# Kernel optimization log

Hardware: AMD Instinct MI355X
Metric: run time of the kernel (lower is better)

The kernel has to match this reference:

```python
import jax, jax.numpy as jnp
import numpy as np

B, S, D = 2, 2048, 2048
H, KV = 32, 8
HD = D // H          # 64
REP = H // KV        # 4


def setup_inputs() -> dict:
    key = jax.random.key(0)
    ks = jax.random.split(key, 7)
    x = jax.random.normal(ks[0], (B, S, D), dtype=jnp.float32)
    # rotary tables: cos/sin of position*inv_freq, shape (S, HD//2)
    inv_freq = 1.0 / (10000.0 ** (np.arange(0, HD, 2, dtype=np.float32) / HD))
    t = np.arange(S, dtype=np.float32)
    freqs = np.outer(t, inv_freq)
    freqs_cos = jnp.asarray(np.cos(freqs))
    freqs_sin = jnp.asarray(np.sin(freqs))
    sc = 0.02
    wq = jax.random.normal(ks[1], (D, D), dtype=jnp.float32) * sc
    wk = jax.random.normal(ks[2], (KV * HD, D), dtype=jnp.float32) * sc
    wv = jax.random.normal(ks[3], (KV * HD, D), dtype=jnp.float32) * sc
    wo = jax.random.normal(ks[4], (D, D), dtype=jnp.float32) * sc
    return {"x": x, "freqs_cos": freqs_cos, "freqs_sin": freqs_sin,
            "wq": wq, "wk": wk, "wv": wv, "wo": wo}


def _rope(t, cos, sin):
    # t: (B, S, h, HD); interleaved real/imag pairs along last dim
    r = t[..., 0::2]
    i = t[..., 1::2]
    cos = cos[None, :, None, :]
    sin = sin[None, :, None, :]
    out_r = r * cos - i * sin
    out_i = r * sin + i * cos
    return jnp.stack([out_r, out_i], axis=-1).reshape(t.shape)


def reference(x, freqs_cos, freqs_sin, wq, wk, wv, wo):
    b, s, d = x.shape
    xq = jnp.einsum('bsd,ed->bse', x, wq).reshape(b, s, H, HD)
    xk = jnp.einsum('bsd,ed->bse', x, wk).reshape(b, s, KV, HD)
    xv = jnp.einsum('bsd,ed->bse', x, wv).reshape(b, s, KV, HD)
    xq = _rope(xq, freqs_cos, freqs_sin)
    xk = _rope(xk, freqs_cos, freqs_sin)
    # GQA repeat_kv: (B,S,KV,HD) -> (B,S,H,HD)
    xk = jnp.repeat(xk, REP, axis=2)
    xv = jnp.repeat(xv, REP, axis=2)
    # to (B,H,S,HD)
    q = xq.transpose(0, 2, 1, 3)
    k = xk.transpose(0, 2, 1, 3)
    v = xv.transpose(0, 2, 1, 3)
    scores = jnp.einsum('bhqd,bhkd->bhqk', q, k) / jnp.sqrt(jnp.float32(HD))
    causal = jnp.tril(jnp.ones((s, s), dtype=bool))
    scores = jnp.where(causal[None, None], scores, jnp.float32(-1e30))
    probs = jax.nn.softmax(scores, axis=-1)
    out = jnp.einsum('bhqk,bhkd->bhqd', probs, v)
    out = out.transpose(0, 2, 1, 3).reshape(b, s, d)
    return jnp.einsum('bsd,ed->bse', out, wo)
```

## Files before the change

### kernel.cpp

```cpp
#include <hip/hip_runtime.h>
#include <cstdint>
#include <cstddef>

#define S_LEN 2048
#define D_MODEL 2048
#define NH 32
#define NKV 8
#define HD_ 64
#define BATCH 2
#define KVD 512
#define MTOT 4096

typedef float f32x4 __attribute__((ext_vector_type(4)));
typedef short s16x8 __attribute__((ext_vector_type(8)));
typedef unsigned int u32;
typedef unsigned int u32x4 __attribute__((ext_vector_type(4)));

__device__ __forceinline__ unsigned short f2bf(float f) {
  unsigned int u = __builtin_bit_cast(unsigned int, f);
  u = (u + 0x7fffu + ((u >> 16) & 1u)) >> 16;
  return (unsigned short)u;
}
__device__ __forceinline__ float bf2f(unsigned short h) {
  return __builtin_bit_cast(float, ((unsigned int)h) << 16);
}
__device__ __forceinline__ float fexp2(float x) {
#if __has_builtin(__builtin_amdgcn_exp2f)
  return __builtin_amdgcn_exp2f(x);
#else
  return exp2f(x);
#endif
}

__device__ __forceinline__ void gl_lds16(const void* g, void* l) {
  __builtin_amdgcn_global_load_lds((const __attribute__((address_space(1))) u32*)g,
                                   (__attribute__((address_space(3))) u32*)l, 16, 0, 0);
}

__global__ void cvt_kernel(const float* __restrict__ in, unsigned short* __restrict__ out, int n4) {
  int i = blockIdx.x * blockDim.x + threadIdx.x;
  if (i >= n4) return;
  float4 v = reinterpret_cast<const float4*>(in)[i];
  ushort4 o;
  o.x = f2bf(v.x); o.y = f2bf(v.y); o.z = f2bf(v.z); o.w = f2bf(v.w);
  reinterpret_cast<ushort4*>(out)[i] = o;
}

__global__ void cvt4_kernel(const float* __restrict__ a, const float* __restrict__ b,
                            const float* __restrict__ c, const float* __restrict__ d,
                            unsigned short* __restrict__ oa, unsigned short* __restrict__ ob,
                            unsigned short* __restrict__ oc, unsigned short* __restrict__ od,
                            int na4, int nb4, int nc4, int nd4) {
  int j = blockIdx.x * blockDim.x + threadIdx.x;
  const float* src; unsigned short* dst;
  if (j < na4) { src = a; dst = oa; }
  else {
    j -= na4;
    if (j < nb4) { src = b; dst = ob; }
    else {
      j -= nb4;
      if (j < nc4) { src = c; dst = oc; }
      else {
        j -= nc4;
        if (j >= nd4) return;
        src = d; dst = od;
      }
    }
  }
  float4 v = reinterpret_cast<const float4*>(src)[j];
  ushort4 o;
  o.x = f2bf(v.x); o.y = f2bf(v.y); o.z = f2bf(v.z); o.w = f2bf(v.w);
  reinterpret_cast<ushort4*>(dst)[j] = o;
}

__global__ void rope2_kernel(unsigned short* __restrict__ qb, unsigned short* __restrict__ kb,
                             const float* __restrict__ cosb, const float* __restrict__ sinb,
                             int totq, int totk, float qscale) {
  int i = blockIdx.x * blockDim.x + threadIdx.x;
  unsigned short* buf; int nheads; float scale;
  if (i < totq) { buf = qb; nheads = NH; scale = qscale; }
  else {
    i -= totq;
    if (i >= totk) return;
    buf = kb; nheads = NKV; scale = 1.0f;
  }
  int pair = i & 31;
  int rest = i >> 5;
  int s = (rest / nheads) % S_LEN;
  float c = cosb[s * 32 + pair], sn = sinb[s * 32 + pair];
  size_t base = (size_t)rest * HD_ + (size_t)pair * 2;
  float r  = bf2f(buf[base]);
  float im = bf2f(buf[base + 1]);
  buf[base]     = f2bf((r * c - im * sn) * scale);
  buf[base + 1] = f2bf((r * sn + im * c) * scale);
}

template<int MODE>
__global__ __launch_bounds__(256) void gemm_bt(const unsigned short* __restrict__ A,
                                               const unsigned short* __restrict__ W,
                                               float* __restrict__ Cf,
                                               unsigned short* __restrict__ Cb,
                                               int M, int N, int K) {
  __shared__ alignas(16) short As[128 * 32];
  __shared__ alignas(16) short Bs[128 * 32];
  int tid = threadIdx.x;
  int lane = tid & 63, wid = tid >> 6;
  int m0 = blockIdx.y * 128;
  int n0 = blockIdx.x * 128;
  int wm = (wid >> 1) * 64, wn = (wid & 1) * 64;
  int lrow = lane & 15, lkk = lane >> 4;
  int srow = lane >> 2;
  int scb  = (lane & 3) * 16;
  f32x4 acc[4][4] = {};

  for (int k0 = 0; k0 < K; k0 += 32) {
    __syncthreads();
#pragma unroll
    for (int i = 0; i < 2; ++i) {
      int c = wid * 2 + i;
      int row = c * 16 + srow;
      const char* ga = (const char*)A + ((size_t)(m0 + row) * K + k0) * 2 + scb;
      gl_lds16(ga, (char*)As + c * 1024);
      const char* gw = (const char*)W + ((size_t)(n0 + row) * K + k0) * 2 + scb;
      gl_lds16(gw, (char*)Bs + c * 1024);
    }
    __syncthreads();
    s16x8 af[4], bfr[4];
#pragma unroll
    for (int mi = 0; mi < 4; ++mi) {
      int row = wm + mi * 16 + lrow;
      af[mi] = *reinterpret_cast<const s16x8*>((const char*)As + row * 64 + lkk * 16);
    }
#pragma unroll
    for (int ni = 0; ni < 4; ++ni) {
      int row = wn + ni * 16 + lrow;
      bfr[ni] = *reinterpret_cast<const s16x8*>((const char*)Bs + row * 64 + lkk * 16);
    }
#pragma unroll
    for (int mi = 0; mi < 4; ++mi)
#pragma unroll
      for (int ni = 0; ni < 4; ++ni)
        acc[mi][ni] = __builtin_amdgcn_mfma_f32_16x16x32_bf16(af[mi], bfr[ni], acc[mi][ni], 0, 0, 0);
  }

#pragma unroll
  for (int mi = 0; mi < 4; ++mi)
#pragma unroll
    for (int ni = 0; ni < 4; ++ni)
#pragma unroll
      for (int r = 0; r < 4; ++r) {
        int row = m0 + wm + mi * 16 + lkk * 4 + r;
        int col = n0 + wn + ni * 16 + lrow;
        if (MODE == 1) Cf[(size_t)row * N + col] = acc[mi][ni][r];
        else           Cb[(size_t)row * N + col] = f2bf(acc[mi][ni][r]);
      }
}

__global__ __launch_bounds__(256) void gemm_kv(const unsigned short* __restrict__ A,
                                               const unsigned short* __restrict__ Wk,
                                               const unsigned short* __restrict__ Wv,
                                               unsigned short* __restrict__ Ck,
                                               unsigned short* __restrict__ Cvt,
                                               int M, int K) {
  __shared__ alignas(16) short As[128 * 32];
  __shared__ alignas(16) short Bs[128 * 32];
  int tid = threadIdx.x;
  int lane = tid & 63, wid = tid >> 6;
  bool isV = blockIdx.x >= 4;
  const unsigned short* W = isV ? Wv : Wk;
  int n0 = (isV ? (int)blockIdx.x - 4 : (int)blockIdx.x) * 128;
  int m0 = blockIdx.y * 128;
  int wm = (wid >> 1) * 64, wn = (wid & 1) * 64;
  int lrow = lane & 15, lkk = lane >> 4;
  int srow = lane >> 2;
  int scb  = (lane & 3) * 16;
  f32x4 acc[4][4] = {};

  for (int k0 = 0; k0 < K; k0 += 32) {
    __syncthreads();
#pragma unroll
    for (int i = 0; i < 2; ++i) {
      int c = wid * 2 + i;
      int row = c * 16 + srow;
      const char* ga = (const char*)A + ((size_t)(m0 + row) * K + k0) * 2 + scb;
      gl_lds16(ga, (char*)As + c * 1024);
      const char* gw = (const char*)W + ((size_t)(n0 + row) * K + k0) * 2 + scb;
      gl_lds16(gw, (char*)Bs + c * 1024);
    }
    __syncthreads();
    s16x8 af[4], bfr[4];
#pragma unroll
    for (int mi = 0; mi < 4; ++mi) {
      int row = wm + mi * 16 + lrow;
      af[mi] = *reinterpret_cast<const s16x8*>((const char*)As + row * 64 + lkk * 16);
    }
#pragma unroll
    for (int ni = 0; ni < 4; ++ni) {
      int row = wn + ni * 16 + lrow;
      bfr[ni] = *reinterpret_cast<const s16x8*>((const char*)Bs + row * 64 + lkk * 16);
    }
#pragma unroll
    for (int mi = 0; mi < 4; ++mi)
#pragma unroll
      for (int ni = 0; ni < 4; ++ni)
        acc[mi][ni] = __builtin_amdgcn_mfma_f32_16x16x32_bf16(af[mi], bfr[ni], acc[mi][ni], 0, 0, 0);
  }

  if (!isV) {
#pragma unroll
    for (int mi = 0; mi < 4; ++mi)
#pragma unroll
      for (int ni = 0; ni < 4; ++ni)
#pragma unroll
        for (int r = 0; r < 4; ++r) {
          int row = m0 + wm + mi * 16 + lkk * 4 + r;
          int col = n0 + wn + ni * 16 + lrow;
          Ck[(size_t)row * KVD + col] = f2bf(acc[mi][ni][r]);
        }
  } else {
#pragma unroll
    for (int mi = 0; mi < 4; ++mi)
#pragma unroll
      for (int ni = 0; ni < 4; ++ni) {
        int col = n0 + wn + ni * 16 + lrow;
        int mrow = m0 + wm + mi * 16 + lkk * 4;
        ushort4 o;
        o.x = f2bf(acc[mi][ni][0]); o.y = f2bf(acc[mi][ni][1]);
        o.z = f2bf(acc[mi][ni][2]); o.w = f2bf(acc[mi][ni][3]);
        *reinterpret_cast<ushort4*>(Cvt + (size_t)col * M + mrow) = o;
      }
  }
}

__global__ __launch_bounds__(256) void attn_kernel(const unsigned short* __restrict__ Q,
                                                   const unsigned short* __restrict__ Kb,
                                                   const unsigned short* __restrict__ Vt,
                                                   unsigned short* __restrict__ O) {
  __shared__ alignas(16) short Ks[2][64 * 64];
  __shared__ alignas(16) short Vs[2][64 * 64];

  int tid = threadIdx.x, lane = tid & 63, wid = tid >> 6;
  int qi = lane & 15, lk = lane >> 4;
  int bh = blockIdx.y;
  int b = bh / NH, h = bh % NH, kvh = h >> 2;
  size_t bS = (size_t)b * S_LEN;
  int srow = tid >> 3;
  int scb  = (tid & 7) * 16;
  int sw0  = (srow & 7) << 4;

  const char* kbG = (const char*)Kb + (bS * KVD + (size_t)kvh * HD_) * 2;
  const char* vtG = (const char*)Vt + ((size_t)(kvh * 64) * MTOT + bS) * 2;

  s16x8 kr0, kr1, vr0, vr1;
  auto GLOAD = [&](int kv0) {
    kr0 = *reinterpret_cast<const s16x8*>(kbG + (size_t)(kv0 + srow) * (KVD * 2) + scb);
    kr1 = *reinterpret_cast<const s16x8*>(kbG + (size_t)(kv0 + srow + 32) * (KVD * 2) + scb);
    vr0 = *reinterpret_cast<const s16x8*>(vtG + (size_t)srow * (MTOT * 2) + kv0 * 2 + scb);
    vr1 = *reinterpret_cast<const s16x8*>(vtG + (size_t)(srow + 32) * (MTOT * 2) + kv0 * 2 + scb);
  };
  auto SWRITE = [&](int bf) {
    *reinterpret_cast<s16x8*>((char*)Ks[bf] + srow * 128 + (scb ^ sw0)) = kr0;
    *reinterpret_cast<s16x8*>((char*)Ks[bf] + (srow + 32) * 128 + (scb ^ sw0)) = kr1;
    *reinterpret_cast<s16x8*>((char*)Vs[bf] + srow * 128 + (scb ^ sw0)) = vr0;
    *reinterpret_cast<s16x8*>((char*)Vs[bf] + (srow + 32) * 128 + (scb ^ sw0)) = vr1;
  };

#pragma unroll 1
  for (int job = 0; job < 2; ++job) {
    int qtile = (job == 0) ? (int)blockIdx.x : 31 - (int)blockIdx.x;
    int q0 = qtile * 64;
    int nt = qtile + 1;

    const unsigned short* qptr = Q + (bS + q0 + wid * 16 + qi) * D_MODEL + h * HD_;
    s16x8 qf0 = *reinterpret_cast<const s16x8*>(qptr + lk * 8);
    s16x8 qf1 = *reinterpret_cast<const s16x8*>(qptr + 32 + lk * 8);

    f32x4 o_acc[4] = {};
    float m_run = -3.0e38f, l_run = 0.f;

    GLOAD(0);
    SWRITE(0);
    __syncthreads();
    int cur = 0;

    for (int t = 0; t < nt; ++t) {
      if (t + 1 < nt) GLOAD((t + 1) * 64);

      const char* kbase = (const char*)Ks[cur];
      const char* vbase = (const char*)Vs[cur];

      f32x4 st[4];
      __builtin_amdgcn_s_setprio(1);
#pragma unroll
      for (int mt = 0; mt < 4; ++mt) {
        int row = mt * 16 + qi;
        int sw = (row & 7) << 4;
        s16x8 ka0 = *reinterpret_cast<const s16x8*>(kbase + row * 128 + ((lk * 16) ^ sw));
        s16x8 ka1 = *reinterpret_cast<const s16x8*>(kbase + row * 128 + ((64 + lk * 16) ^ sw));
        f32x4 a = {};
        a = __builtin_amdgcn_mfma_f32_16x16x32_bf16(ka0, qf0, a, 0, 0, 0);
        a = __builtin_amdgcn_mfma_f32_16x16x32_bf16(ka1, qf1, a, 0, 0, 0);
        st[mt] = a;
      }
      __builtin_amdgcn_s_setprio(0);

      if (t == nt - 1) {
        int ql = wid * 16 + qi;
#pragma unroll
        for (int mt = 0; mt < 4; ++mt)
#pragma unroll
          for (int r = 0; r < 4; ++r) {
            int kvl = mt * 16 + 4 * lk + r;
            if (kvl > ql) st[mt][r] = -3.0e38f;
          }
      }

      float pmax = st[0][0];
#pragma unroll
      for (int mt = 0; mt < 4; ++mt)
#pragma unroll
        for (int r = 0; r < 4; ++r) pmax = fmaxf(pmax, st[mt][r]);
      pmax = fmaxf(pmax, __shfl_xor(pmax, 16, 64));
      pmax = fmaxf(pmax, __shfl_xor(pmax, 32, 64));
      float mnew = fmaxf(m_run, pmax);
      float alpha = fexp2(m_run - mnew);
      m_run = mnew;
      float psum = 0.f;
#pragma unroll
      for (int mt = 0; mt < 4; ++mt)
#pragma unroll
        for (int r = 0; r < 4; ++r) {
          float p = fexp2(st[mt][r] - mnew);
          st[mt][r] = p;
          psum += p;
        }
      psum += __shfl_xor(psum, 16, 64);
      psum += __shfl_xor(psum, 32, 64);
      l_run = l_run * alpha + psum;

      u32 pk[4][2];
#pragma unroll
      for (int mt = 0; mt < 4; ++mt)
#pragma unroll
        for (int w = 0; w < 2; ++w)
          pk[mt][w] = (u32)f2bf(st[mt][2 * w]) | ((u32)f2bf(st[mt][2 * w + 1]) << 16);

      float ar[4];
#pragma unroll
      for (int r = 0; r < 4; ++r) ar[r] = __shfl(alpha, 4 * lk + r, 64);
#pragma unroll
      for (int n = 0; n < 4; ++n)
#pragma unroll
        for (int r = 0; r < 4; ++r) o_acc[n][r] *= ar[r];

      int s0 = qi + 32 * (lk & 1);
      int s2 = s0 + 16;
      bool hiw = lk >= 2;
      s16x8 pa[2];
#pragma unroll
      for (int ks = 0; ks < 2; ++ks) {
        u32 a0 = (u32)__shfl((int)pk[2 * ks][0], s0, 64), b0 = (u32)__shfl((int)pk[2 * ks + 1][0], s0, 64);
        u32 a1 = (u32)__shfl((int)pk[2 * ks][1], s0, 64), b1 = (u32)__shfl((int)pk[2 * ks + 1][1], s0, 64);
        u32 a2 = (u32)__shfl((int)pk[2 * ks][0], s2, 64), b2 = (u32)__shfl((int)pk[2 * ks + 1][0], s2, 64);
        u32 a3 = (u32)__shfl((int)pk[2 * ks][1], s2, 64), b3 = (u32)__shfl((int)pk[2 * ks + 1][1], s2, 64);
        u32x4 wv_;
        wv_[0] = hiw ? b0 : a0; wv_[1] = hiw ? b1 : a1;
        wv_[2] = hiw ? b2 : a2; wv_[3] = hiw ? b3 : a3;
        pa[ks] = __builtin_bit_cast(s16x8, wv_);
      }

      __builtin_amdgcn_s_setprio(1);
#pragma unroll
      for (int n = 0; n < 4; ++n) {
        int vr = n * 16 + qi;
        int sw = (vr & 7) << 4;
        s16x8 vb0 = *reinterpret_cast<const s16x8*>(vbase + vr * 128 + ((lk * 16) ^ sw));
        s16x8 vb1 = *reinterpret_cast<const s16x8*>(vbase + vr * 128 + ((64 + lk * 16) ^ sw));
        o_acc[n] = __builtin_amdgcn_mfma_f32_16x16x32_bf16(pa[0], vb0, o_acc[n], 0, 0, 0);
        o_acc[n] = __builtin_amdgcn_mfma_f32_16x16x32_bf16(pa[1], vb1, o_acc[n], 0, 0, 0);
      }
      __builtin_amdgcn_s_setprio(0);

      if (t + 1 < nt) SWRITE(cur ^ 1);
      __syncthreads();
      cur ^= 1;
    }

    float linv[4];
#pragma unroll
    for (int r = 0; r < 4; ++r) linv[r] = 1.0f / __shfl(l_run, 4 * lk + r, 64);
#pragma unroll
    for (int n = 0; n < 4; ++n)
#pragma unroll
      for (int r = 0; r < 4; ++r) {
        size_t row = bS + q0 + wid * 16 + 4 * lk + r;
        int col = h * HD_ + n * 16 + qi;
        O[row * D_MODEL + col] = f2bf(o_acc[n][r] * linv[r]);
      }
  }
}

extern "C" void kernel_launch(void* const* d_in, const int* in_sizes, int n_in,
                              void* d_out, int out_size, void* d_ws, size_t ws_size,
                              hipStream_t stream) {
  const float* x  = (const float*)d_in[0];
  const float* fc = (const float*)d_in[1];
  const float* fs = (const float*)d_in[2];
  const float* wq = (const float*)d_in[3];
  const float* wk = (const float*)d_in[4];
  const float* wv = (const float*)d_in[5];
  const float* wo = (const float*)d_in[6];
  float* out = (float*)d_out;

  const size_t nx  = (size_t)BATCH * S_LEN * D_MODEL;
  const size_t nw  = (size_t)D_MODEL * D_MODEL;
  const size_t nwk = (size_t)KVD * D_MODEL;
  const size_t nkv = (size_t)BATCH * S_LEN * KVD;

  char* ws = (char*)d_ws;
  unsigned short* xb  = (unsigned short*)ws;  ws += nx  * 2;
  unsigned short* wqb = (unsigned short*)ws;  ws += nw  * 2;
  unsigned short* wkb = (unsigned short*)ws;  ws += nwk * 2;
  unsigned short* wvb = (unsigned short*)ws;  ws += nwk * 2;
  unsigned short* wob = (unsigned short*)ws;  ws += nw  * 2;
  unsigned short* qb  = (unsigned short*)ws;  ws += nx  * 2;
  unsigned short* kb  = (unsigned short*)ws;  ws += nkv * 2;
  unsigned short* vtb = (unsigned short*)ws;  ws += nkv * 2;
  unsigned short* ab  = (unsigned short*)ws;  ws += nx  * 2;

  cvt_kernel<<<dim3((nx / 4 + 255) / 256), dim3(256), 0, stream>>>(x, xb, nx / 4);
  {
    int na4 = nw / 4, nb4 = nwk / 4, nc4 = nwk / 4, nd4 = nw / 4;
    int tot = na4 + nb4 + nc4 + nd4;
    cvt4_kernel<<<dim3((tot + 255) / 256), dim3(256), 0, stream>>>(wq, wk, wv, wo, wqb, wkb, wvb, wob,
                                                                   na4, nb4, nc4, nd4);
  }

  const int M = BATCH * S_LEN;
  gemm_bt<0><<<dim3(D_MODEL / 128, M / 128), dim3(256), 0, stream>>>(xb, wqb, nullptr, qb, M, D_MODEL, D_MODEL);
  gemm_kv<<<dim3(8, M / 128), dim3(256), 0, stream>>>(xb, wkb, wvb, kb, vtb, M, D_MODEL);

  {
    int totq = BATCH * S_LEN * NH * 32;
    int totk = BATCH * S_LEN * NKV * 32;
    rope2_kernel<<<dim3((totq + totk + 255) / 256), dim3(256), 0, stream>>>(qb, kb, fc, fs, totq, totk,
                                                                            0.18033688011112042f);
  }

  attn_kernel<<<dim3(16, BATCH * NH), dim3(256), 0, stream>>>(qb, kb, vtb, ab);

  gemm_bt<1><<<dim3(D_MODEL / 128, M / 128), dim3(256), 0, stream>>>(ab, wob, out, nullptr, M, D_MODEL, D_MODEL);
}
```

Baseline: 392.4 us.

## Fuse QKV GEMMs and enlarge attention query tiles with lazy rescaling

Merges the Q projection and the K/V projection GEMMs into a single launch with 24 column-block groups. The attention kernel moves to 512 threads per block and 128-row query tiles, so each K/V tile loaded into shared memory serves twice as many queries, while warps skip tiles that lie entirely past their causal limit. It also adds a lazy online-softmax rescale that only updates the running max when it grows by more than a threshold. The risks are higher register and occupancy pressure from the larger blocks, warp divergence at the diagonal, and subtle numerical effects from the deferred rescaling.

Result: faster. 336.3 us (-14.3%).

```diff
diff --git a/kernel.cpp b/kernel.cpp
--- a/kernel.cpp
+++ b/kernel.cpp
@@ -95,12 +95,92 @@
   buf[base + 1] = f2bf((r * sn + im * c) * scale);
 }
 
-template<int MODE>
-__global__ __launch_bounds__(256) void gemm_bt(const unsigned short* __restrict__ A,
-                                               const unsigned short* __restrict__ W,
-                                               float* __restrict__ Cf,
-                                               unsigned short* __restrict__ Cb,
-                                               int M, int N, int K) {
+__global__ __launch_bounds__(256) void gemm_qkv(const unsigned short* __restrict__ A,
+                                                const unsigned short* __restrict__ Wq,
+                                                const unsigned short* __restrict__ Wk,
+                                                const unsigned short* __restrict__ Wv,
+                                                unsigned short* __restrict__ Cq,
+                                                unsigned short* __restrict__ Ck,
+                                                unsigned short* __restrict__ Cvt,
+                                                int M, int K) {
+  __shared__ alignas(16) short As[128 * 32];
+  __shared__ alignas(16) short Bs[128 * 32];
+  int tid = threadIdx.x;
+  int lane = tid & 63, wid = tid >> 6;
+  int bx = blockIdx.x;
+  const unsigned short* W; int n0, mode;
+  if (bx < 16)      { W = Wq; n0 = bx * 128;        mode = 0; }
+  else if (bx < 20) { W = Wk; n0 = (bx - 16) * 128; mode = 1; }
+  else              { W = Wv; n0 = (bx - 20) * 128; mode = 2; }
+  int m0 = blockIdx.y * 128;
+  int wm = (wid >> 1) * 64, wn = (wid & 1) * 64;
+  int lrow = lane & 15, lkk = lane >> 4;
+  int srow = lane >> 2;
+  int scb  = (lane & 3) * 16;
+  f32x4 acc[4][4] = {};
+
+  for (int k0 = 0; k0 < K; k0 += 32) {
+    __syncthreads();
+#pragma unroll
+    for (int i = 0; i < 2; ++i) {
+      int c = wid * 2 + i;
+      int row = c * 16 + srow;
+      const char* ga = (const char*)A + ((size_t)(m0 + row) * K + k0) * 2 + scb;
+      gl_lds16(ga, (char*)As + c * 1024);
+      const char* gw = (const char*)W + ((size_t)(n0 + row) * K + k0) * 2 + scb;
+      gl_lds16(gw, (char*)Bs + c * 1024);
+    }
+    __syncthreads();
+    s16x8 af[4], bfr[4];
+#pragma unroll
+    for (int mi = 0; mi < 4; ++mi) {
+      int row = wm + mi * 16 + lrow;
+      af[mi] = *reinterpret_cast<const s16x8*>((const char*)As + row * 64 + lkk * 16);
+    }
+#pragma unroll
+    for (int ni = 0; ni < 4; ++ni) {
+      int row = wn + ni * 16 + lrow;
+      bfr[ni] = *reinterpret_cast<const s16x8*>((const char*)Bs + row * 64 + lkk * 16);
+    }
+#pragma unroll
+    for (int mi = 0; mi < 4; ++mi)
+#pragma unroll
+      for (int ni = 0; ni < 4; ++ni)
+        acc[mi][ni] = __builtin_amdgcn_mfma_f32_16x16x32_bf16(af[mi], bfr[ni], acc[mi][ni], 0, 0, 0);
+  }
+
+  if (mode == 2) {
+#pragma unroll
+    for (int mi = 0; mi < 4; ++mi)
+#pragma unroll
+      for (int ni = 0; ni < 4; ++ni) {
+        int col = n0 + wn + ni * 16 + lrow;
+        int mrow = m0 + wm + mi * 16 + lkk * 4;
+        ushort4 o;
+        o.x = f2bf(acc[mi][ni][0]); o.y = f2bf(acc[mi][ni][1]);
+        o.z = f2bf(acc[mi][ni][2]); o.w = f2bf(acc[mi][ni][3]);
+        *reinterpret_cast<ushort4*>(Cvt + (size_t)col * M + mrow) = o;
+      }
+  } else {
+    unsigned short* C = (mode == 0) ? Cq : Ck;
+    int N = (mode == 0) ? D_MODEL : KVD;
+#pragma unroll
+    for (int mi = 0; mi < 4; ++mi)
+#pragma unroll
+      for (int ni = 0; ni < 4; ++ni)
+#pragma unroll
+        for (int r = 0; r < 4; ++r) {
+          int row = m0 + wm + mi * 16 + lkk * 4 + r;
+          int col = n0 + wn + ni * 16 + lrow;
+          C[(size_t)row * N + col] = f2bf(acc[mi][ni][r]);
+        }
+  }
+}
+
+__global__ __launch_bounds__(256) void gemm_out(const unsigned short* __restrict__ A,
+                                                const unsigned short* __restrict__ W,
+                                                float* __restrict__ Cf,
+                                                int M, int N, int K) {
   __shared__ alignas(16) short As[128 * 32];
   __shared__ alignas(16) short Bs[128 * 32];
   int tid = threadIdx.x;
@@ -151,88 +231,11 @@
       for (int r = 0; r < 4; ++r) {
         int row = m0 + wm + mi * 16 + lkk * 4 + r;
         int col = n0 + wn + ni * 16 + lrow;
-        if (MODE == 1) Cf[(size_t)row * N + col] = acc[mi][ni][r];
-        else           Cb[(size_t)row * N + col] = f2bf(acc[mi][ni][r]);
+        Cf[(size_t)row * N + col] = acc[mi][ni][r];
       }
 }
 
-__global__ __launch_bounds__(256) void gemm_kv(const unsigned short* __restrict__ A,
-                                               const unsigned short* __restrict__ Wk,
-                                               const unsigned short* __restrict__ Wv,
-                                               unsigned short* __restrict__ Ck,
-                                               unsigned short* __restrict__ Cvt,
-                                               int M, int K) {
-  __shared__ alignas(16) short As[128 * 32];
-  __shared__ alignas(16) short Bs[128 * 32];
-  int tid = threadIdx.x;
-  int lane = tid & 63, wid = tid >> 6;
-  bool isV = blockIdx.x >= 4;
-  const unsigned short* W = isV ? Wv : Wk;
-  int n0 = (isV ? (int)blockIdx.x - 4 : (int)blockIdx.x) * 128;
-  int m0 = blockIdx.y * 128;
-  int wm = (wid >> 1) * 64, wn = (wid & 1) * 64;
-  int lrow = lane & 15, lkk = lane >> 4;
-  int srow = lane >> 2;
-  int scb  = (lane & 3) * 16;
-  f32x4 acc[4][4] = {};
-
-  for (int k0 = 0; k0 < K; k0 += 32) {
-    __syncthreads();
-#pragma unroll
-    for (int i = 0; i < 2; ++i) {
-      int c = wid * 2 + i;
-      int row = c * 16 + srow;
-      const char* ga = (const char*)A + ((size_t)(m0 + row) * K + k0) * 2 + scb;
-      gl_lds16(ga, (char*)As + c * 1024);
-      const char* gw = (const char*)W + ((size_t)(n0 + row) * K + k0) * 2 + scb;
-      gl_lds16(gw, (char*)Bs + c * 1024);
-    }
-    __syncthreads();
-    s16x8 af[4], bfr[4];
-#pragma unroll
-    for (int mi = 0; mi < 4; ++mi) {
-      int row = wm + mi * 16 + lrow;
-      af[mi] = *reinterpret_cast<const s16x8*>((const char*)As + row * 64 + lkk * 16);
-    }
-#pragma unroll
-    for (int ni = 0; ni < 4; ++ni) {
-      int row = wn + ni * 16 + lrow;
-      bfr[ni] = *reinterpret_cast<const s16x8*>((const char*)Bs + row * 64 + lkk * 16);
-    }
-#pragma unroll
-    for (int mi = 0; mi < 4; ++mi)
-#pragma unroll
-      for (int ni = 0; ni < 4; ++ni)
-        acc[mi][ni] = __builtin_amdgcn_mfma_f32_16x16x32_bf16(af[mi], bfr[ni], acc[mi][ni], 0, 0, 0);
-  }
-
-  if (!isV) {
-#pragma unroll
-    for (int mi = 0; mi < 4; ++mi)
-#pragma unroll
-      for (int ni = 0; ni < 4; ++ni)
-#pragma unroll
-        for (int r = 0; r < 4; ++r) {
-          int row = m0 + wm + mi * 16 + lkk * 4 + r;
-          int col = n0 + wn + ni * 16 + lrow;
-          Ck[(size_t)row * KVD + col] = f2bf(acc[mi][ni][r]);
-        }
-  } else {
-#pragma unroll
-    for (int mi = 0; mi < 4; ++mi)
-#pragma unroll
-      for (int ni = 0; ni < 4; ++ni) {
-        int col = n0 + wn + ni * 16 + lrow;
-        int mrow = m0 + wm + mi * 16 + lkk * 4;
-        ushort4 o;
-        o.x = f2bf(acc[mi][ni][0]); o.y = f2bf(acc[mi][ni][1]);
-        o.z = f2bf(acc[mi][ni][2]); o.w = f2bf(acc[mi][ni][3]);
-        *reinterpret_cast<ushort4*>(Cvt + (size_t)col * M + mrow) = o;
-      }
-  }
-}
-
-__global__ __launch_bounds__(256) void attn_kernel(const unsigned short* __restrict__ Q,
+__global__ __launch_bounds__(512) void attn_kernel(const unsigned short* __restrict__ Q,
                                                    const unsigned short* __restrict__ Kb,
                                                    const unsigned short* __restrict__ Vt,
                                                    unsigned short* __restrict__ O) {
@@ -251,25 +254,22 @@
   const char* kbG = (const char*)Kb + (bS * KVD + (size_t)kvh * HD_) * 2;
   const char* vtG = (const char*)Vt + ((size_t)(kvh * 64) * MTOT + bS) * 2;
 
-  s16x8 kr0, kr1, vr0, vr1;
+  s16x8 kr, vr;
   auto GLOAD = [&](int kv0) {
-    kr0 = *reinterpret_cast<const s16x8*>(kbG + (size_t)(kv0 + srow) * (KVD * 2) + scb);
-    kr1 = *reinterpret_cast<const s16x8*>(kbG + (size_t)(kv0 + srow + 32) * (KVD * 2) + scb);
-    vr0 = *reinterpret_cast<const s16x8*>(vtG + (size_t)srow * (MTOT * 2) + kv0 * 2 + scb);
-    vr1 = *reinterpret_cast<const s16x8*>(vtG + (size_t)(srow + 32) * (MTOT * 2) + kv0 * 2 + scb);
+    kr = *reinterpret_cast<const s16x8*>(kbG + (size_t)(kv0 + srow) * (KVD * 2) + scb);
+    vr = *reinterpret_cast<const s16x8*>(vtG + (size_t)srow * (MTOT * 2) + kv0 * 2 + scb);
   };
   auto SWRITE = [&](int bf) {
-    *reinterpret_cast<s16x8*>((char*)Ks[bf] + srow * 128 + (scb ^ sw0)) = kr0;
-    *reinterpret_cast<s16x8*>((char*)Ks[bf] + (srow + 32) * 128 + (scb ^ sw0)) = kr1;
-    *reinterpret_cast<s16x8*>((char*)Vs[bf] + srow * 128 + (scb ^ sw0)) = vr0;
-    *reinterpret_cast<s16x8*>((char*)Vs[bf] + (srow + 32) * 128 + (scb ^ sw0)) = vr1;
+    *reinterpret_cast<s16x8*>((char*)Ks[bf] + srow * 128 + (scb ^ sw0)) = kr;
+    *reinterpret_cast<s16x8*>((char*)Vs[bf] + srow * 128 + (scb ^ sw0)) = vr;
   };
 
 #pragma unroll 1
   for (int job = 0; job < 2; ++job) {
-    int qtile = (job == 0) ? (int)blockIdx.x : 31 - (int)blockIdx.x;
-    int q0 = qtile * 64;
-    int nt = qtile + 1;
+    int qtile = (job == 0) ? (int)blockIdx.x : 15 - (int)blockIdx.x;
+    int q0 = qtile * 128;
+    int nt = 2 * qtile + 2;
+    int qlmax = q0 + wid * 16 + 15;
 
     const unsigned short* qptr = Q + (bS + q0 + wid * 16 + qi) * D_MODEL + h * HD_;
     s16x8 qf0 = *reinterpret_cast<const s16x8*>(qptr + lk * 8);
@@ -286,100 +286,106 @@
     for (int t = 0; t < nt; ++t) {
       if (t + 1 < nt) GLOAD((t + 1) * 64);
 
-      const char* kbase = (const char*)Ks[cur];
-      const char* vbase = (const char*)Vs[cur];
-
-      f32x4 st[4];
-      __builtin_amdgcn_s_setprio(1);
-#pragma unroll
-      for (int mt = 0; mt < 4; ++mt) {
-        int row = mt * 16 + qi;
-        int sw = (row & 7) << 4;
-        s16x8 ka0 = *reinterpret_cast<const s16x8*>(kbase + row * 128 + ((lk * 16) ^ sw));
-        s16x8 ka1 = *reinterpret_cast<const s16x8*>(kbase + row * 128 + ((64 + lk * 16) ^ sw));
-        f32x4 a = {};
-        a = __builtin_amdgcn_mfma_f32_16x16x32_bf16(ka0, qf0, a, 0, 0, 0);
-        a = __builtin_amdgcn_mfma_f32_16x16x32_bf16(ka1, qf1, a, 0, 0, 0);
-        st[mt] = a;
+      if (64 * t <= qlmax) {
+        const char* kbase = (const char*)Ks[cur];
+        const char* vbase = (const char*)Vs[cur];
+
+        f32x4 st[4];
+        __builtin_amdgcn_s_setprio(1);
+#pragma unroll
+        for (int mt = 0; mt < 4; ++mt) {
+          int row = mt * 16 + qi;
+          int sw = (row & 7) << 4;
+          s16x8 ka0 = *reinterpret_cast<const s16x8*>(kbase + row * 128 + ((lk * 16) ^ sw));
+          s16x8 ka1 = *reinterpret_cast<const s16x8*>(kbase + row * 128 + ((64 + lk * 16) ^ sw));
+          f32x4 a = {};
+          a = __builtin_amdgcn_mfma_f32_16x16x32_bf16(ka0, qf0, a, 0, 0, 0);
+          a = __builtin_amdgcn_mfma_f32_16x16x32_bf16(ka1, qf1, a, 0, 0, 0);
+          st[mt] = a;
+        }
+        __builtin_amdgcn_s_setprio(0);
+
+        if (t >= nt - 2) {
+          int ql = q0 + wid * 16 + qi;
+#pragma unroll
+          for (int mt = 0; mt < 4; ++mt)
+#pragma unroll
+            for (int r = 0; r < 4; ++r) {
+              int kvg = 64 * t + mt * 16 + 4 * lk + r;
+              if (kvg > ql) st[mt][r] = -3.0e38f;
+            }
+        }
+
+        float pmax = st[0][0];
+#pragma unroll
+        for (int mt = 0; mt < 4; ++mt)
+#pragma unroll
+          for (int r = 0; r < 4; ++r) pmax = fmaxf(pmax, st[mt][r]);
+        pmax = fmaxf(pmax, __shfl_xor(pmax, 16, 64));
+        pmax = fmaxf(pmax, __shfl_xor(pmax, 32, 64));
+
+        if (!__all(pmax <= m_run + 8.0f)) {
+          float mnew = fmaxf(m_run, pmax);
+          float alpha = fexp2(m_run - mnew);
+          m_run = mnew;
+          l_run *= alpha;
+          float ar[4];
+#pragma unroll
+          for (int r = 0; r < 4; ++r) ar[r] = __shfl(alpha, 4 * lk + r, 64);
+#pragma unroll
+          for (int n = 0; n < 4; ++n)
+#pragma unroll
+            for (int r = 0; r < 4; ++r) o_acc[n][r] *= ar[r];
+        }
+
+        float psum = 0.f;
+#pragma unroll
+        for (int mt = 0; mt < 4; ++mt)
+#pragma unroll
+          for (int r = 0; r < 4; ++r) {
+            float p = fexp2(st[mt][r] - m_run);
+            st[mt][r] = p;
+            psum += p;
+          }
+        psum += __shfl_xor(psum, 16, 64);
+        psum += __shfl_xor(psum, 32, 64);
+        l_run += psum;
+
+        u32 pk[4][2];
+#pragma unroll
+        for (int mt = 0; mt < 4; ++mt)
+#pragma unroll
+          for (int w = 0; w < 2; ++w)
+            pk[mt][w] = (u32)f2bf(st[mt][2 * w]) | ((u32)f2bf(st[mt][2 * w + 1]) << 16);
+
+        int s0 = qi + 32 * (lk & 1);
+        int s2 = s0 + 16;
+        bool hiw = lk >= 2;
+        s16x8 pa[2];
+#pragma unroll
+        for (int ks = 0; ks < 2; ++ks) {
+          u32 a0 = (u32)__shfl((int)pk[2 * ks][0], s0, 64), b0 = (u32)__shfl((int)pk[2 * ks + 1][0], s0, 64);
+          u32 a1 = (u32)__shfl((int)pk[2 * ks][1], s0, 64), b1 = (u32)__shfl((int)pk[2 * ks + 1][1], s0, 64);
+          u32 a2 = (u32)__shfl((int)pk[2 * ks][0], s2, 64), b2 = (u32)__shfl((int)pk[2 * ks + 1][0], s2, 64);
+          u32 a3 = (u32)__shfl((int)pk[2 * ks][1], s2, 64), b3 = (u32)__shfl((int)pk[2 * ks + 1][1], s2, 64);
+          u32x4 wv_;
+          wv_[0] = hiw ? b0 : a0; wv_[1] = hiw ? b1 : a1;
+          wv_[2] = hiw ? b2 : a2; wv_[3] = hiw ? b3 : a3;
+          pa[ks] = __builtin_bit_cast(s16x8, wv_);
+        }
+
+        __builtin_amdgcn_s_setprio(1);
+#pragma unroll
+        for (int n = 0; n < 4; ++n) {
+          int vrw = n * 16 + qi;
+          int sw = (vrw & 7) << 4;
+          s16x8 vb0 = *reinterpret_cast<const s16x8*>(vbase + vrw * 128 + ((lk * 16) ^ sw));
+          s16x8 vb1 = *reinterpret_cast<const s16x8*>(vbase + vrw * 128 + ((64 + lk * 16) ^ sw));
+          o_acc[n] = __builtin_amdgcn_mfma_f32_16x16x32_bf16(pa[0], vb0, o_acc[n], 0, 0, 0);
+          o_acc[n] = __builtin_amdgcn_mfma_f32_16x16x32_bf16(pa[1], vb1, o_acc[n], 0, 0, 0);
+        }
+        __builtin_amdgcn_s_setprio(0);
       }
-      __builtin_amdgcn_s_setprio(0);
-
-      if (t == nt - 1) {
-        int ql = wid * 16 + qi;
-#pragma unroll
-        for (int mt = 0; mt < 4; ++mt)
-#pragma unroll
-          for (int r = 0; r < 4; ++r) {
-            int kvl = mt * 16 + 4 * lk + r;
-            if (kvl > ql) st[mt][r] = -3.0e38f;
-          }
-      }
-
-      float pmax = st[0][0];
-#pragma unroll
-      for (int mt = 0; mt < 4; ++mt)
-#pragma unroll
-        for (int r = 0; r < 4; ++r) pmax = fmaxf(pmax, st[mt][r]);
-      pmax = fmaxf(pmax, __shfl_xor(pmax, 16, 64));
-      pmax = fmaxf(pmax, __shfl_xor(pmax, 32, 64));
-      float mnew = fmaxf(m_run, pmax);
-      float alpha = fexp2(m_run - mnew);
-      m_run = mnew;
-      float psum = 0.f;
-#pragma unroll
-      for (int mt = 0; mt < 4; ++mt)
-#pragma unroll
-        for (int r = 0; r < 4; ++r) {
-          float p = fexp2(st[mt][r] - mnew);
-          st[mt][r] = p;
-          psum += p;
-        }
-      psum += __shfl_xor(psum, 16, 64);
-      psum += __shfl_xor(psum, 32, 64);
-      l_run = l_run * alpha + psum;
-
-      u32 pk[4][2];
-#pragma unroll
-      for (int mt = 0; mt < 4; ++mt)
-#pragma unroll
-        for (int w = 0; w < 2; ++w)
-          pk[mt][w] = (u32)f2bf(st[mt][2 * w]) | ((u32)f2bf(st[mt][2 * w + 1]) << 16);
-
-      float ar[4];
-#pragma unroll
-      for (int r = 0; r < 4; ++r) ar[r] = __shfl(alpha, 4 * lk + r, 64);
-#pragma unroll
-      for (int n = 0; n < 4; ++n)
-#pragma unroll
-        for (int r = 0; r < 4; ++r) o_acc[n][r] *= ar[r];
-
-      int s0 = qi + 32 * (lk & 1);
-      int s2 = s0 + 16;
-      bool hiw = lk >= 2;
-      s16x8 pa[2];
-#pragma unroll
-      for (int ks = 0; ks < 2; ++ks) {
-        u32 a0 = (u32)__shfl((int)pk[2 * ks][0], s0, 64), b0 = (u32)__shfl((int)pk[2 * ks + 1][0], s0, 64);
-        u32 a1 = (u32)__shfl((int)pk[2 * ks][1], s0, 64), b1 = (u32)__shfl((int)pk[2 * ks + 1][1], s0, 64);
-        u32 a2 = (u32)__shfl((int)pk[2 * ks][0], s2, 64), b2 = (u32)__shfl((int)pk[2 * ks + 1][0], s2, 64);
-        u32 a3 = (u32)__shfl((int)pk[2 * ks][1], s2, 64), b3 = (u32)__shfl((int)pk[2 * ks + 1][1], s2, 64);
-        u32x4 wv_;
-        wv_[0] = hiw ? b0 : a0; wv_[1] = hiw ? b1 : a1;
-        wv_[2] = hiw ? b2 : a2; wv_[3] = hiw ? b3 : a3;
-        pa[ks] = __builtin_bit_cast(s16x8, wv_);
-      }
-
-      __builtin_amdgcn_s_setprio(1);
-#pragma unroll
-      for (int n = 0; n < 4; ++n) {
-        int vr = n * 16 + qi;
-        int sw = (vr & 7) << 4;
-        s16x8 vb0 = *reinterpret_cast<const s16x8*>(vbase + vr * 128 + ((lk * 16) ^ sw));
-        s16x8 vb1 = *reinterpret_cast<const s16x8*>(vbase + vr * 128 + ((64 + lk * 16) ^ sw));
-        o_acc[n] = __builtin_amdgcn_mfma_f32_16x16x32_bf16(pa[0], vb0, o_acc[n], 0, 0, 0);
-        o_acc[n] = __builtin_amdgcn_mfma_f32_16x16x32_bf16(pa[1], vb1, o_acc[n], 0, 0, 0);
-      }
-      __builtin_amdgcn_s_setprio(0);
 
       if (t + 1 < nt) SWRITE(cur ^ 1);
       __syncthreads();
@@ -437,8 +443,7 @@
   }
 
   const int M = BATCH * S_LEN;
-  gemm_bt<0><<<dim3(D_MODEL / 128, M / 128), dim3(256), 0, stream>>>(xb, wqb, nullptr, qb, M, D_MODEL, D_MODEL);
-  gemm_kv<<<dim3(8, M / 128), dim3(256), 0, stream>>>(xb, wkb, wvb, kb, vtb, M, D_MODEL);
+  gemm_qkv<<<dim3(24, M / 128), dim3(256), 0, stream>>>(xb, wqb, wkb, wvb, qb, kb, vtb, M, D_MODEL);
 
   {
     int totq = BATCH * S_LEN * NH * 32;
@@ -447,7 +452,7 @@
                                                                             0.18033688011112042f);
   }
 
-  attn_kernel<<<dim3(16, BATCH * NH), dim3(256), 0, stream>>>(qb, kb, vtb, ab);
-
-  gemm_bt<1><<<dim3(D_MODEL / 128, M / 128), dim3(256), 0, stream>>>(ab, wob, out, nullptr, M, D_MODEL, D_MODEL);
-}
+  attn_kernel<<<dim3(8, BATCH * NH), dim3(512), 0, stream>>>(qb, kb, vtb, ab);
+
+  gemm_out<<<dim3(D_MODEL / 128, M / 128), dim3(256), 0, stream>>>(ab, wob, out, M, D_MODEL, D_MODEL);
+}
```
